# Kernel optimization log

Hardware: AMD Instinct MI355X
Metric: run time of the kernel (lower is better)

## Reference

```python
import jax, jax.numpy as jnp
import numpy as np

K = 7      # kernel_size
PAD = 3    # padding ('same' with stride 1)
G = 16     # groups


def _unfold(x):
    """torch nn.Unfold equivalent, stride=1, dilation=1.
    Returns [B, C, K*K, H, W] with kernel positions ordered (kh, kw),
    matching torch's (c, kh, kw) channel-major layout after reshape."""
    B, C, H, W = x.shape
    xp = jnp.pad(x, ((0, 0), (0, 0), (PAD, PAD), (PAD, PAD)))
    patches = jnp.stack(
        [xp[:, :, i:i + H, j:j + W] for i in range(K) for j in range(K)],
        axis=2,
    )
    return patches


def setup_inputs() -> dict:
    key = jax.random.key(0)
    k1, k2, k3 = jax.random.split(key, 3)
    B, C, H, W = 4, 256, 64, 64
    x = jax.random.normal(k1, (B, C, H, W), dtype=jnp.float32)
    # 1x1 conv producing kernel_prod*groups = 49*16 = 784 channels (with bias)
    w_kernel = jax.random.normal(k2, (G * K * K, C), dtype=jnp.float32) * 0.05
    b_kernel = jax.random.normal(k3, (G * K * K,), dtype=jnp.float32) * 0.05
    return {"x": x, "w_kernel": w_kernel, "b_kernel": b_kernel}


def reference(x, w_kernel, b_kernel):
    B, C, H, W = x.shape
    Cg = C // G
    # unfolded input: [B, G, C//G, K*K, H, W]
    patches = _unfold(x).reshape(B, G, Cg, K * K, H, W)
    # dynamic per-pixel kernel: AvgPool(k=1) is identity at stride 1,
    # then 1x1 conv with bias -> [B, G*K*K, H, W]
    kern = jnp.einsum('bchw,kc->bkhw', x, w_kernel) + b_kernel[None, :, None, None]
    kern = kern.reshape(B, G, 1, K * K, H, W)
    # multiply and sum-reduce over kernel positions, flatten groups
    out = (patches * kern).sum(axis=3).reshape(B, C, H, W)
    return out
```

## Files before the change

kernel.cpp:

```cpp
#include <hip/hip_runtime.h>


#define B_   4
#define C_   256
#define G_   16
#define KK_  49
#define KS_  7
#define PD_  3

#define XT_BYTES  (B_*4096*C_*2)
#define WBF_OFF   XT_BYTES

#define SKW   28
#define HR_   71
#define HCPS  (10*HR_)

typedef __attribute__((ext_vector_type(8))) short bf16x8;
typedef __attribute__((ext_vector_type(4))) float f32x4;
typedef unsigned short ushort_t;

__device__ inline unsigned f2bf(float f) {
    unsigned u = __float_as_uint(f);
    u += 0x7FFF + ((u >> 16) & 1);
    return u >> 16;
}

__global__ __launch_bounds__(256)
void cvt_xT(const float* __restrict__ x, const float* __restrict__ wk,
            ushort_t* __restrict__ xT, unsigned* __restrict__ wbf) {
    const int t = threadIdx.x;
    if (blockIdx.x == 64) {
        const int slice = blockIdx.z * 4 + blockIdx.y;
        const float2* wk2 = (const float2*)wk;
        const int base = slice * 6272;
        for (int k = t; k < 6272; k += 256) {
            float2 v = wk2[base + k];
            wbf[base + k] = f2bf(v.x) | (f2bf(v.y) << 16);
        }
        return;
    }
    __shared__ float tile[64][65];
    const int p0 = blockIdx.x * 64;
    const int c0 = blockIdx.y * 64;
    const int b  = blockIdx.z;
    const int px_r = t & 63;
    #pragma unroll
    for (int i = 0; i < 16; ++i) {
        int ch = (t >> 6) + i * 4;
        tile[ch][px_r] = x[((size_t)(b * C_ + c0 + ch) << 12) + p0 + px_r];
    }
    __syncthreads();
    const int px  = t >> 2;
    const int seg = t & 3;
    unsigned u[8];
    #pragma unroll
    for (int j = 0; j < 8; ++j) {
        float a0 = tile[seg * 16 + 2 * j][px];
        float a1 = tile[seg * 16 + 2 * j + 1][px];
        u[j] = f2bf(a0) | (f2bf(a1) << 16);
    }
    unsigned* dst = (unsigned*)(xT + ((size_t)((b << 12) + p0 + px)) * C_ + c0 + seg * 16);
    ((uint4*)dst)[0] = make_uint4(u[0], u[1], u[2], u[3]);
    ((uint4*)dst)[1] = make_uint4(u[4], u[5], u[6], u[7]);
}

__global__ __launch_bounds__(256, 4)
void inv_fused(const ushort_t* __restrict__ xT,
               const ushort_t* __restrict__ wbf,
               const float* __restrict__ bk,
               const float* __restrict__ x,
               float* __restrict__ out) {
    __shared__ unsigned kern2[256 * SKW];
    __shared__ unsigned halo2[4 * HCPS];

    const int bid  = blockIdx.x;
    const int g    = bid >> 6;
    const int b    = (bid >> 4) & 3;
    const int tile = bid & 15;
    const int gy0  = tile * 4;
    const int p0   = gy0 * 64;

    const int tid  = threadIdx.x;
    const int wv   = tid >> 6;
    const int ln15 = tid & 15;
    const int quad = (tid & 63) >> 4;

    f32x4 acc[16];
    #pragma unroll
    for (int i = 0; i < 16; ++i) acc[i] = (f32x4){0.f, 0.f, 0.f, 0.f};

    const ushort_t* ap[4];
    #pragma unroll
    for (int mt = 0; mt < 4; ++mt) {
        int r = mt * 16 + ln15; if (r > KK_ - 1) r = KK_ - 1;
        ap[mt] = wbf + (size_t)(g * KK_ + r) * C_ + quad * 8;
    }
    const ushort_t* bp = xT + ((size_t)((b << 12) + p0 + wv * 64 + ln15)) * C_ + quad * 8;

    bf16x8 af[2][4], bf[2][4];
    #pragma unroll
    for (int mt = 0; mt < 4; ++mt) af[0][mt] = *(const bf16x8*)(ap[mt]);
    #pragma unroll
    for (int nt = 0; nt < 4; ++nt) bf[0][nt] = *(const bf16x8*)(bp + nt * 16 * C_);

    #pragma unroll
    for (int k = 0; k < 8; ++k) {
        const int cur = k & 1, nxt = cur ^ 1;
        if (k < 7) {
            const int cc = (k + 1) * 32;
            #pragma unroll
            for (int mt = 0; mt < 4; ++mt)
                af[nxt][mt] = *(const bf16x8*)(ap[mt] + cc);
            #pragma unroll
            for (int nt = 0; nt < 4; ++nt)
                bf[nxt][nt] = *(const bf16x8*)(bp + nt * 16 * C_ + cc);
        }
        #pragma unroll
        for (int mt = 0; mt < 4; ++mt) {
            #pragma unroll
            for (int nt = 0; nt < 4; ++nt) {
                acc[mt * 4 + nt] = __builtin_amdgcn_mfma_f32_16x16x32_bf16(
                    af[cur][mt], bf[cur][nt], acc[mt * 4 + nt], 0, 0, 0);
            }
        }
    }

    #pragma unroll
    for (int mt = 0; mt < 3; ++mt) {
        const int m0 = mt * 16 + quad * 4;
        const float b0 = bk[g * KK_ + m0],     b1 = bk[g * KK_ + m0 + 1];
        const float b2 = bk[g * KK_ + m0 + 2], b3 = bk[g * KK_ + m0 + 3];
        #pragma unroll
        for (int nt = 0; nt < 4; ++nt) {
            const int p = wv * 64 + nt * 16 + ln15;
            uint2 d;
            d.x = f2bf(acc[mt * 4 + nt][0] + b0) | (f2bf(acc[mt * 4 + nt][1] + b1) << 16);
            d.y = f2bf(acc[mt * 4 + nt][2] + b2) | (f2bf(acc[mt * 4 + nt][3] + b3) << 16);
            *(uint2*)&kern2[p * SKW + mt * 8 + quad * 2] = d;
        }
    }
    if (quad == 0) {
        const float b48 = bk[g * KK_ + 48];
        #pragma unroll
        for (int nt = 0; nt < 4; ++nt) {
            const int p = wv * 64 + nt * 16 + ln15;
            kern2[p * SKW + 24] = f2bf(acc[12 + nt][0] + b48);
        }
    }
    __syncthreads();

    float kv[KK_];
    {
        const uint4* kr = (const uint4*)&kern2[tid * SKW];
        unsigned kd[28];
        #pragma unroll
        for (int q = 0; q < 7; ++q) {
            uint4 h = kr[q];
            kd[4*q] = h.x; kd[4*q+1] = h.y; kd[4*q+2] = h.z; kd[4*q+3] = h.w;
        }
        #pragma unroll
        for (int k = 0; k < KK_; ++k) {
            unsigned d = kd[k >> 1];
            kv[k] = __uint_as_float((k & 1) ? (d & 0xffff0000u) : (d << 16));
        }
    }

    const int py = tid >> 6, px = tid & 63;
    #pragma unroll 1
    for (int hb = 0; hb < 2; ++hb) {
        if (hb) __syncthreads();
        const int cbase = g * 16 + hb * 8;
        for (int e = tid; e < 4 * HCPS; e += 256) {
            int cp  = e / HCPS;
            int rem = e - cp * HCPS;
            int row = rem / HR_;
            int col = rem - row * HR_;
            int sy = gy0 + row - PD_;
            int sx = col - PD_;
            float v0 = 0.f, v1 = 0.f;
            if (sy >= 0 && sy < 64 && sx >= 0 && sx < 64) {
                const float* xp = x + ((size_t)(b * C_ + cbase + 2 * cp) << 12) + sy * 64 + sx;
                v0 = xp[0];
                v1 = xp[4096];
            }
            halo2[e] = f2bf(v0) | (f2bf(v1) << 16);
        }
        __syncthreads();

        #pragma unroll 1
        for (int cp = 0; cp < 4; ++cp) {
            float a0 = 0.f, a1 = 0.f;
            #pragma unroll
            for (int kh = 0; kh < KS_; ++kh) {
                const unsigned* hr = &halo2[cp * HCPS + (py + kh) * HR_ + px];
                #pragma unroll
                for (int kw = 0; kw < KS_; ++kw) {
                    unsigned d = hr[kw];
                    float kk = kv[kh * KS_ + kw];
                    a0 = fmaf(__uint_as_float(d << 16),          kk, a0);
                    a1 = fmaf(__uint_as_float(d & 0xffff0000u),  kk, a1);
                }
            }
            size_t o = ((size_t)(b * C_ + cbase + 2 * cp) << 12) + p0 + tid;
            out[o] = a0;
            out[o + 4096] = a1;
        }
    }
}

extern "C" void kernel_launch(void* const* d_in, const int* in_sizes, int n_in,
                              void* d_out, int out_size, void* d_ws, size_t ws_size,
                              hipStream_t stream) {
    const float* x  = (const float*)d_in[0];
    const float* wk = (const float*)d_in[1];
    const float* bk = (const float*)d_in[2];
    float* o = (float*)d_out;

    ushort_t* xT  = (ushort_t*)d_ws;
    unsigned* wbf = (unsigned*)((char*)d_ws + WBF_OFF);

    cvt_xT<<<dim3(65, 4, B_), dim3(256), 0, stream>>>(x, wk, xT, wbf);
    inv_fused<<<dim3(1024), dim3(256), 0, stream>>>(
        xT, (const ushort_t*)wbf, bk, x, o);
}
```

Baseline: 128.0 us.

## Interleave eight channels per halo position for vectorized LDS reads

The halo tile layout changes from two bf16 channels per word, stored channel-pair-major, to eight bf16 channels packed into a uint4 per spatial position. The aggregation loop then does one 128-bit LDS read per tap and updates eight accumulators, instead of looping over four channel pairs with 32-bit reads. This cuts LDS instruction count and loop overhead. In exchange, register pressure rises and the 16-byte stride per position may cause bank conflicts on the uint4 reads.

```diff
diff --git a/kernel.cpp b/kernel.cpp
--- a/kernel.cpp
+++ b/kernel.cpp
@@ -12,8 +12,8 @@
 #define WBF_OFF   XT_BYTES
 
 #define SKW   28
-#define HR_   71
-#define HCPS  (10*HR_)
+#define HC_   70
+#define HPOS  (10*HC_)
 
 typedef __attribute__((ext_vector_type(8))) short bf16x8;
 typedef __attribute__((ext_vector_type(4))) float f32x4;
@@ -71,7 +71,7 @@
                const float* __restrict__ x,
                float* __restrict__ out) {
     __shared__ unsigned kern2[256 * SKW];
-    __shared__ unsigned halo2[4 * HCPS];
+    __shared__ unsigned halo4[HPOS * 4];
 
     const int bid  = blockIdx.x;
     const int g    = bid >> 6;
@@ -170,41 +170,47 @@
     for (int hb = 0; hb < 2; ++hb) {
         if (hb) __syncthreads();
         const int cbase = g * 16 + hb * 8;
-        for (int e = tid; e < 4 * HCPS; e += 256) {
-            int cp  = e / HCPS;
-            int rem = e - cp * HCPS;
-            int row = rem / HR_;
-            int col = rem - row * HR_;
+        for (int e = tid; e < HPOS; e += 256) {
+            int row = e / HC_;
+            int col = e - row * HC_;
             int sy = gy0 + row - PD_;
             int sx = col - PD_;
-            float v0 = 0.f, v1 = 0.f;
+            unsigned d0 = 0, d1 = 0, d2 = 0, d3 = 0;
             if (sy >= 0 && sy < 64 && sx >= 0 && sx < 64) {
-                const float* xp = x + ((size_t)(b * C_ + cbase + 2 * cp) << 12) + sy * 64 + sx;
-                v0 = xp[0];
-                v1 = xp[4096];
+                const float* xp = x + ((size_t)(b * C_ + cbase) << 12) + sy * 64 + sx;
+                d0 = f2bf(xp[0])             | (f2bf(xp[1 << 12]) << 16);
+                d1 = f2bf(xp[2 << 12])       | (f2bf(xp[3 << 12]) << 16);
+                d2 = f2bf(xp[4 << 12])       | (f2bf(xp[5 << 12]) << 16);
+                d3 = f2bf(xp[6 << 12])       | (f2bf(xp[7 << 12]) << 16);
             }
-            halo2[e] = f2bf(v0) | (f2bf(v1) << 16);
+            *(uint4*)&halo4[e * 4] = make_uint4(d0, d1, d2, d3);
         }
         __syncthreads();
 
-        #pragma unroll 1
-        for (int cp = 0; cp < 4; ++cp) {
-            float a0 = 0.f, a1 = 0.f;
-            #pragma unroll
-            for (int kh = 0; kh < KS_; ++kh) {
-                const unsigned* hr = &halo2[cp * HCPS + (py + kh) * HR_ + px];
-                #pragma unroll
-                for (int kw = 0; kw < KS_; ++kw) {
-                    unsigned d = hr[kw];
-                    float kk = kv[kh * KS_ + kw];
-                    a0 = fmaf(__uint_as_float(d << 16),          kk, a0);
-                    a1 = fmaf(__uint_as_float(d & 0xffff0000u),  kk, a1);
-                }
+        float a[8];
+        #pragma unroll
+        for (int q = 0; q < 8; ++q) a[q] = 0.f;
+        #pragma unroll
+        for (int kh = 0; kh < KS_; ++kh) {
+            const uint4* hr = (const uint4*)&halo4[(((py + kh) * HC_) + px) * 4];
+            #pragma unroll
+            for (int kw = 0; kw < KS_; ++kw) {
+                uint4 hv = hr[kw];
+                float kk = kv[kh * KS_ + kw];
+                a[0] = fmaf(__uint_as_float(hv.x << 16),          kk, a[0]);
+                a[1] = fmaf(__uint_as_float(hv.x & 0xffff0000u),  kk, a[1]);
+                a[2] = fmaf(__uint_as_float(hv.y << 16),          kk, a[2]);
+                a[3] = fmaf(__uint_as_float(hv.y & 0xffff0000u),  kk, a[3]);
+                a[4] = fmaf(__uint_as_float(hv.z << 16),          kk, a[4]);
+                a[5] = fmaf(__uint_as_float(hv.z & 0xffff0000u),  kk, a[5]);
+                a[6] = fmaf(__uint_as_float(hv.w << 16),          kk, a[6]);
+                a[7] = fmaf(__uint_as_float(hv.w & 0xffff0000u),  kk, a[7]);
             }
-            size_t o = ((size_t)(b * C_ + cbase + 2 * cp) << 12) + p0 + tid;
-            out[o] = a0;
-            out[o + 4096] = a1;
-        }
+        }
+        const size_t o = ((size_t)(b * C_ + cbase) << 12) + p0 + tid;
+        #pragma unroll
+        for (int q = 0; q < 8; ++q)
+            out[o + ((size_t)q << 12)] = a[q];
     }
 }
 
```

Result: faster. 117.7 us (-8.1%).
